# Optimization experiments

Measured on AMD Instinct MI355X. Metric: run time of the kernel, lower is better.

The kernel has to match this reference:

```python
import jax, jax.numpy as jnp
import numpy as np


def _prelu(x, a):
    # torch.nn.PReLU with per-channel parameter a (broadcast over batch)
    return jnp.where(x >= 0, x, a * x)


def setup_inputs() -> dict:
    key = jax.random.key(0)
    ks = jax.random.split(key, 12)
    B = 8192
    dims = [512, 1024, 1024, 512]  # tardim
    E = 8                          # tctrl = modim[-1]
    scale = 0.02                   # keep activations well-scaled across 3 layers
    inp = {
        "x": jax.random.normal(ks[0], (B, dims[0]), dtype=jnp.float32),
        "weights": jax.random.uniform(ks[1], (E,), dtype=jnp.float32),
    }
    for i in range(3):
        din, dout = dims[i], dims[i + 1]
        inp[f"W{i}"] = jax.random.normal(ks[2 + 3 * i], (E, din, dout), dtype=jnp.float32) * scale
        inp[f"b{i}"] = jax.random.normal(ks[3 + 3 * i], (E, dout), dtype=jnp.float32) * scale
        inp[f"a{i}"] = jnp.full((dout,), 0.25, dtype=jnp.float32)  # PReLU init
    return inp


def reference(x, weights, W0, b0, a0, W1, b1, a1, W2, b2, a2):
    # mie.g: per layer, weighted sum over tctrl expert Linears, then PReLU.
    # sum_j (w_j/sum(w)) * (x @ W_j + b_j) == x @ (sum_j wn_j W_j) + sum_j wn_j b_j,
    # so pre-merge expert weights (tiny contraction) and do one GEMM per layer.
    wn = weights / jnp.sum(weights)  # [E]
    for W, b, a in ((W0, b0, a0), (W1, b1, a1), (W2, b2, a2)):
        Wm = jnp.einsum('e,eio->io', wn, W)  # merged weight [in, out]
        bm = jnp.einsum('e,eo->o', wn, b)    # merged bias   [out]
        x = _prelu(x @ Wm + bm, a)           # [B, out]
    return x
```

## Files before the change

kernel.cpp:

```cpp
#include <hip/hip_runtime.h>
#include <stdint.h>

typedef unsigned short u16;
typedef __attribute__((ext_vector_type(8))) short short8;
typedef __attribute__((ext_vector_type(4))) float float4v;

__device__ __forceinline__ u16 f2bf(float f) {
    union { float f; uint32_t u; } v; v.f = f;
    uint32_t r = v.u + 0x7fffu + ((v.u >> 16) & 1u);
    return (u16)(r >> 16);
}

__device__ __forceinline__ void gload16(const u16* g, u16* l) {
    __builtin_amdgcn_global_load_lds(
        (const __attribute__((address_space(1))) void*)g,
        (__attribute__((address_space(3))) void*)l, 16, 0, 0);
}

__global__ __launch_bounds__(256) void prep_fused(
    const float* __restrict__ x, u16* __restrict__ xbf,
    const float* __restrict__ wts,
    const float* __restrict__ W0, const float* __restrict__ W1, const float* __restrict__ W2,
    u16* __restrict__ W0t, u16* __restrict__ W1t, u16* __restrict__ W2t,
    const float* __restrict__ b0, const float* __restrict__ b1, const float* __restrict__ b2,
    float* __restrict__ bm) {
    __shared__ float tile[32][33];
    const int b = blockIdx.x, tid = threadIdx.x;

    if (b < 4096) {
        int i = (b * 256 + tid) * 4;
        float4 v = *(const float4*)(x + i);
        union { u16 s[4]; uint64_t q; } o;
        o.s[0] = f2bf(v.x); o.s[1] = f2bf(v.y); o.s[2] = f2bf(v.z); o.s[3] = f2bf(v.w);
        *(uint64_t*)(xbf + i) = o.q;
        return;
    }

    float wn[8]; float s = 0.f;
    #pragma unroll
    for (int e = 0; e < 8; ++e) { wn[e] = wts[e]; s += wn[e]; }
    const float inv = 1.0f / s;

    if (b < 6144) {
        const float* W; u16* Wt; int K, N, lb;
        if (b < 4608)      { W = W0; Wt = W0t; K = 512;  N = 1024; lb = b - 4096; }
        else if (b < 5632) { W = W1; Wt = W1t; K = 1024; N = 1024; lb = b - 4608; }
        else               { W = W2; Wt = W2t; K = 1024; N = 512;  lb = b - 5632; }
        const int ntiles = N >> 5;
        const int o0 = (lb % ntiles) * 32, i0 = (lb / ntiles) * 32;
        const int tx = tid & 31, ty = tid >> 5;
        #pragma unroll
        for (int s4 = 0; s4 < 4; ++s4) {
            int il = ty + s4 * 8;
            float acc = 0.f;
            #pragma unroll
            for (int e = 0; e < 8; ++e)
                acc += wn[e] * W[(size_t)e * K * N + (size_t)(i0 + il) * N + o0 + tx];
            tile[il][tx] = acc * inv;
        }
        __syncthreads();
        #pragma unroll
        for (int s4 = 0; s4 < 4; ++s4) {
            int ol = ty + s4 * 8;
            Wt[(size_t)(o0 + ol) * K + i0 + tx] = f2bf(tile[tx][ol]);
        }
        return;
    }

    int t = (b - 6144) * 256 + tid;
    if (t >= 2560) return;
    const float* bp; int o, stride;
    if (t < 1024)      { bp = b0; o = t;        stride = 1024; }
    else if (t < 2048) { bp = b1; o = t - 1024; stride = 1024; }
    else               { bp = b2; o = t - 2048; stride = 512;  }
    float acc = 0.f;
    #pragma unroll
    for (int e = 0; e < 8; ++e) acc += wn[e] * bp[e * stride + o];
    bm[t] = acc * inv;
}

template <bool OUT_F32>
__global__ __launch_bounds__(256, 4) void gemm_bias_prelu(
    const u16* __restrict__ A, const u16* __restrict__ Bt,
    const float* __restrict__ bias, const float* __restrict__ alpha,
    void* __restrict__ outp, int M, int N, int K) {
    __shared__ __align__(16) u16 As[128 * 64];
    __shared__ __align__(16) u16 Bs[64 * 64];
    const int tid = threadIdx.x;
    const int bn = blockIdx.x, bm = blockIdx.y;

    const int r0 = tid >> 3;
    const int p  = tid & 7;
    const int c  = p ^ (r0 & 7);
    const u16* Ag = A  + (size_t)(bm * 128 + r0) * K + c * 8;
    const u16* Bg = Bt + (size_t)(bn * 64  + r0) * K + c * 8;
    u16* Al = As + tid * 8;
    u16* Bl = Bs + tid * 8;

    const int lane = tid & 63, w = tid >> 6;
    const int wm = (w >> 1) * 64, wncol = (w & 1) * 32;
    const int l16 = lane & 15, quad = lane >> 4;
    const int xr = l16 & 7;
    const short8* As8 = (const short8*)As;
    const short8* Bs8 = (const short8*)Bs;

    float4v acc[4][2] = {};

    const int nk = K >> 6;
    for (int kt = 0; kt < nk; ++kt) {
        #pragma unroll
        for (int it = 0; it < 4; ++it)
            gload16(Ag + (size_t)(it * 32) * K, Al + it * 2048);
        #pragma unroll
        for (int it = 0; it < 2; ++it)
            gload16(Bg + (size_t)(it * 32) * K, Bl + it * 2048);
        __syncthreads();
        #pragma unroll
        for (int kk = 0; kk < 2; ++kk) {
            const int cb = kk * 4;
            short8 af[4], bf[2];
            #pragma unroll
            for (int mi = 0; mi < 4; ++mi)
                af[mi] = As8[(wm + mi * 16 + l16) * 8 + ((cb + quad) ^ xr)];
            #pragma unroll
            for (int ni = 0; ni < 2; ++ni)
                bf[ni] = Bs8[(wncol + ni * 16 + l16) * 8 + ((cb + quad) ^ xr)];
            #pragma unroll
            for (int mi = 0; mi < 4; ++mi)
                #pragma unroll
                for (int ni = 0; ni < 2; ++ni)
                    acc[mi][ni] = __builtin_amdgcn_mfma_f32_16x16x32_bf16(
                        af[mi], bf[ni], acc[mi][ni], 0, 0, 0);
        }
        if (kt + 1 < nk) __syncthreads();
        Ag += 64; Bg += 64;
    }

    const int cbase = bn * 64 + wncol + l16;
    float bv[2], av[2];
    #pragma unroll
    for (int ni = 0; ni < 2; ++ni) { bv[ni] = bias[cbase + ni * 16]; av[ni] = alpha[cbase + ni * 16]; }
    const int rbase = bm * 128 + wm + quad * 4;
    #pragma unroll
    for (int mi = 0; mi < 4; ++mi) {
        #pragma unroll
        for (int reg = 0; reg < 4; ++reg) {
            int r = rbase + mi * 16 + reg;
            #pragma unroll
            for (int ni = 0; ni < 2; ++ni) {
                float v = acc[mi][ni][reg] + bv[ni];
                v = v >= 0.f ? v : av[ni] * v;
                size_t idx = (size_t)r * N + cbase + ni * 16;
                if (OUT_F32) ((float*)outp)[idx] = v;
                else         ((u16*)outp)[idx] = f2bf(v);
            }
        }
    }
}

extern "C" void kernel_launch(void* const* d_in, const int* in_sizes, int n_in,
                              void* d_out, int out_size, void* d_ws, size_t ws_size,
                              hipStream_t stream) {
    const float* x   = (const float*)d_in[0];
    const float* wts = (const float*)d_in[1];
    const float* W0  = (const float*)d_in[2];
    const float* b0  = (const float*)d_in[3];
    const float* a0  = (const float*)d_in[4];
    const float* W1  = (const float*)d_in[5];
    const float* b1  = (const float*)d_in[6];
    const float* a1  = (const float*)d_in[7];
    const float* W2  = (const float*)d_in[8];
    const float* b2  = (const float*)d_in[9];
    const float* a2  = (const float*)d_in[10];
    float* out = (float*)d_out;

    char* ws = (char*)d_ws;
    u16*   xbf  = (u16*)ws;  ws += (size_t)8192 * 512 * 2;
    u16*   act1 = (u16*)ws;  ws += (size_t)8192 * 1024 * 2;
    u16*   act2 = (u16*)ws;  ws += (size_t)8192 * 1024 * 2;
    u16*   W0t  = (u16*)ws;  ws += (size_t)1024 * 512 * 2;
    u16*   W1t  = (u16*)ws;  ws += (size_t)1024 * 1024 * 2;
    u16*   W2t  = (u16*)ws;  ws += (size_t)512 * 1024 * 2;
    float* bm   = (float*)ws;

    prep_fused<<<6154, 256, 0, stream>>>(x, xbf, wts, W0, W1, W2, W0t, W1t, W2t,
                                         b0, b1, b2, bm);

    gemm_bias_prelu<false><<<dim3(16, 64), 256, 0, stream>>>(xbf,  W0t, bm,        a0, act1, 8192, 1024, 512);
    gemm_bias_prelu<false><<<dim3(16, 64), 256, 0, stream>>>(act1, W1t, bm + 1024, a1, act2, 8192, 1024, 1024);
    gemm_bias_prelu<true ><<<dim3(8, 64),  256, 0, stream>>>(act2, W2t, bm + 2048, a2, out,  8192, 512, 1024);
}
```

Measured before the change: 196.4 us.

## Fuse prep and three GEMM layers into one cooperative persistent kernel

Replaces the four separate launches with a single cooperative kernel of 512 blocks that runs the prep phase and then the three GEMM layers, separated by grid-wide syncs. GEMM tiles grow to 128x128 with 512 threads, so one block covers one output tile per layer and no work loop is needed. This is meant to remove launch gaps and tail effects between kernels. In exchange, a fixed grid of 512 gives exactly one wave with no load balancing, layer 3 leaves half the blocks idle, and the prep phase now runs on far fewer blocks. A non-cooperative fallback path is kept.

```diff
diff --git a/kernel.cpp b/kernel.cpp
--- a/kernel.cpp
+++ b/kernel.cpp
@@ -1,5 +1,8 @@
 #include <hip/hip_runtime.h>
+#include <hip/hip_cooperative_groups.h>
 #include <stdint.h>
+
+namespace cg = cooperative_groups;
 
 typedef unsigned short u16;
 typedef __attribute__((ext_vector_type(8))) short short8;
@@ -17,88 +20,82 @@
         (__attribute__((address_space(3))) void*)l, 16, 0, 0);
 }
 
-__global__ __launch_bounds__(256) void prep_fused(
-    const float* __restrict__ x, u16* __restrict__ xbf,
-    const float* __restrict__ wts,
-    const float* __restrict__ W0, const float* __restrict__ W1, const float* __restrict__ W2,
-    u16* __restrict__ W0t, u16* __restrict__ W1t, u16* __restrict__ W2t,
-    const float* __restrict__ b0, const float* __restrict__ b1, const float* __restrict__ b2,
-    float* __restrict__ bm) {
-    __shared__ float tile[32][33];
-    const int b = blockIdx.x, tid = threadIdx.x;
-
-    if (b < 4096) {
-        int i = (b * 256 + tid) * 4;
-        float4 v = *(const float4*)(x + i);
+struct Params {
+    const float *x, *wts, *W0, *b0, *a0, *W1, *b1, *a1, *W2, *b2, *a2;
+    u16 *xbf, *act1, *act2, *W0t, *W1t, *W2t;
+    float *mb;
+    float *out;
+};
+
+__device__ void prep_phase(const Params& p, int bid, int tid, float (*tile)[33]) {
+    for (int i = (bid * 512 + tid) * 4; i < 8192 * 512; i += 512 * 512 * 4) {
+        float4 v = *(const float4*)(p.x + i);
         union { u16 s[4]; uint64_t q; } o;
         o.s[0] = f2bf(v.x); o.s[1] = f2bf(v.y); o.s[2] = f2bf(v.z); o.s[3] = f2bf(v.w);
-        *(uint64_t*)(xbf + i) = o.q;
-        return;
-    }
-
-    float wn[8]; float s = 0.f;
+        *(uint64_t*)(p.xbf + i) = o.q;
+    }
+
+    float wnv[8]; float ssum = 0.f;
     #pragma unroll
-    for (int e = 0; e < 8; ++e) { wn[e] = wts[e]; s += wn[e]; }
-    const float inv = 1.0f / s;
-
-    if (b < 6144) {
+    for (int e = 0; e < 8; ++e) { wnv[e] = p.wts[e]; ssum += wnv[e]; }
+    const float inv = 1.0f / ssum;
+
+    for (int u = bid; u < 2048; u += 512) {
         const float* W; u16* Wt; int K, N, lb;
-        if (b < 4608)      { W = W0; Wt = W0t; K = 512;  N = 1024; lb = b - 4096; }
-        else if (b < 5632) { W = W1; Wt = W1t; K = 1024; N = 1024; lb = b - 4608; }
-        else               { W = W2; Wt = W2t; K = 1024; N = 512;  lb = b - 5632; }
-        const int ntiles = N >> 5;
-        const int o0 = (lb % ntiles) * 32, i0 = (lb / ntiles) * 32;
+        if (u < 512)       { W = p.W0; Wt = p.W0t; K = 512;  N = 1024; lb = u; }
+        else if (u < 1536) { W = p.W1; Wt = p.W1t; K = 1024; N = 1024; lb = u - 512; }
+        else               { W = p.W2; Wt = p.W2t; K = 1024; N = 512;  lb = u - 1536; }
+        const int nt = N >> 5;
+        const int o0 = (lb % nt) * 32, i0 = (lb / nt) * 32;
         const int tx = tid & 31, ty = tid >> 5;
-        #pragma unroll
-        for (int s4 = 0; s4 < 4; ++s4) {
-            int il = ty + s4 * 8;
+        __syncthreads();
+        #pragma unroll
+        for (int s4 = 0; s4 < 2; ++s4) {
+            int il = ty + s4 * 16;
             float acc = 0.f;
             #pragma unroll
             for (int e = 0; e < 8; ++e)
-                acc += wn[e] * W[(size_t)e * K * N + (size_t)(i0 + il) * N + o0 + tx];
+                acc += wnv[e] * W[(size_t)e * K * N + (size_t)(i0 + il) * N + o0 + tx];
             tile[il][tx] = acc * inv;
         }
         __syncthreads();
         #pragma unroll
-        for (int s4 = 0; s4 < 4; ++s4) {
-            int ol = ty + s4 * 8;
+        for (int s4 = 0; s4 < 2; ++s4) {
+            int ol = ty + s4 * 16;
             Wt[(size_t)(o0 + ol) * K + i0 + tx] = f2bf(tile[tx][ol]);
         }
-        return;
-    }
-
-    int t = (b - 6144) * 256 + tid;
-    if (t >= 2560) return;
-    const float* bp; int o, stride;
-    if (t < 1024)      { bp = b0; o = t;        stride = 1024; }
-    else if (t < 2048) { bp = b1; o = t - 1024; stride = 1024; }
-    else               { bp = b2; o = t - 2048; stride = 512;  }
-    float acc = 0.f;
-    #pragma unroll
-    for (int e = 0; e < 8; ++e) acc += wn[e] * bp[e * stride + o];
-    bm[t] = acc * inv;
+    }
+
+    if (bid < 5) {
+        int t = bid * 512 + tid;
+        if (t < 2560) {
+            const float* bp; int o, stride;
+            if (t < 1024)      { bp = p.b0; o = t;        stride = 1024; }
+            else if (t < 2048) { bp = p.b1; o = t - 1024; stride = 1024; }
+            else               { bp = p.b2; o = t - 2048; stride = 512;  }
+            float acc = 0.f;
+            #pragma unroll
+            for (int e = 0; e < 8; ++e) acc += wnv[e] * bp[e * stride + o];
+            p.mb[t] = acc * inv;
+        }
+    }
 }
 
 template <bool OUT_F32>
-__global__ __launch_bounds__(256, 4) void gemm_bias_prelu(
-    const u16* __restrict__ A, const u16* __restrict__ Bt,
-    const float* __restrict__ bias, const float* __restrict__ alpha,
-    void* __restrict__ outp, int M, int N, int K) {
-    __shared__ __align__(16) u16 As[128 * 64];
-    __shared__ __align__(16) u16 Bs[64 * 64];
-    const int tid = threadIdx.x;
-    const int bn = blockIdx.x, bm = blockIdx.y;
-
+__device__ void gemm_tile(const u16* __restrict__ A, const u16* __restrict__ Bt,
+                          const float* __restrict__ bias, const float* __restrict__ alpha,
+                          void* __restrict__ outp, int N, int K, int bn, int bmi,
+                          u16* As, u16* Bs, int tid) {
     const int r0 = tid >> 3;
     const int p  = tid & 7;
     const int c  = p ^ (r0 & 7);
-    const u16* Ag = A  + (size_t)(bm * 128 + r0) * K + c * 8;
-    const u16* Bg = Bt + (size_t)(bn * 64  + r0) * K + c * 8;
+    const u16* Ag = A  + (size_t)(bmi * 128 + r0) * K + c * 8;
+    const u16* Bg = Bt + (size_t)(bn * 128 + r0) * K + c * 8;
     u16* Al = As + tid * 8;
     u16* Bl = Bs + tid * 8;
 
     const int lane = tid & 63, w = tid >> 6;
-    const int wm = (w >> 1) * 64, wncol = (w & 1) * 32;
+    const int wm = (w >> 2) * 64, wn = (w & 3) * 32;
     const int l16 = lane & 15, quad = lane >> 4;
     const int xr = l16 & 7;
     const short8* As8 = (const short8*)As;
@@ -108,12 +105,10 @@
 
     const int nk = K >> 6;
     for (int kt = 0; kt < nk; ++kt) {
-        #pragma unroll
-        for (int it = 0; it < 4; ++it)
-            gload16(Ag + (size_t)(it * 32) * K, Al + it * 2048);
-        #pragma unroll
-        for (int it = 0; it < 2; ++it)
-            gload16(Bg + (size_t)(it * 32) * K, Bl + it * 2048);
+        gload16(Ag, Al);
+        gload16(Ag + (size_t)64 * K, Al + 4096);
+        gload16(Bg, Bl);
+        gload16(Bg + (size_t)64 * K, Bl + 4096);
         __syncthreads();
         #pragma unroll
         for (int kk = 0; kk < 2; ++kk) {
@@ -124,7 +119,7 @@
                 af[mi] = As8[(wm + mi * 16 + l16) * 8 + ((cb + quad) ^ xr)];
             #pragma unroll
             for (int ni = 0; ni < 2; ++ni)
-                bf[ni] = Bs8[(wncol + ni * 16 + l16) * 8 + ((cb + quad) ^ xr)];
+                bf[ni] = Bs8[(wn + ni * 16 + l16) * 8 + ((cb + quad) ^ xr)];
             #pragma unroll
             for (int mi = 0; mi < 4; ++mi)
                 #pragma unroll
@@ -132,15 +127,15 @@
                     acc[mi][ni] = __builtin_amdgcn_mfma_f32_16x16x32_bf16(
                         af[mi], bf[ni], acc[mi][ni], 0, 0, 0);
         }
-        if (kt + 1 < nk) __syncthreads();
+        __syncthreads();
         Ag += 64; Bg += 64;
     }
 
-    const int cbase = bn * 64 + wncol + l16;
+    const int cbase = bn * 128 + wn + l16;
     float bv[2], av[2];
     #pragma unroll
     for (int ni = 0; ni < 2; ++ni) { bv[ni] = bias[cbase + ni * 16]; av[ni] = alpha[cbase + ni * 16]; }
-    const int rbase = bm * 128 + wm + quad * 4;
+    const int rbase = bmi * 128 + wm + quad * 4;
     #pragma unroll
     for (int mi = 0; mi < 4; ++mi) {
         #pragma unroll
@@ -158,22 +153,47 @@
     }
 }
 
+__global__ __launch_bounds__(512, 4) void fused(Params p) {
+    __shared__ __align__(16) u16 smem[2 * 128 * 64];
+    const int tid = threadIdx.x, bid = blockIdx.x;
+    cg::grid_group grid = cg::this_grid();
+
+    prep_phase(p, bid, tid, (float(*)[33])smem);
+    __threadfence();
+    grid.sync();
+
+    u16* As = smem;
+    u16* Bs = smem + 128 * 64;
+
+    gemm_tile<false>(p.xbf, p.W0t, p.mb, p.a0, p.act1, 1024, 512, bid >> 6, bid & 63, As, Bs, tid);
+    __threadfence();
+    grid.sync();
+
+    gemm_tile<false>(p.act1, p.W1t, p.mb + 1024, p.a1, p.act2, 1024, 1024, bid >> 6, bid & 63, As, Bs, tid);
+    __threadfence();
+    grid.sync();
+
+    if (bid < 256)
+        gemm_tile<true>(p.act2, p.W2t, p.mb + 2048, p.a2, p.out, 512, 1024, bid >> 6, bid & 63, As, Bs, tid);
+}
+
+__global__ __launch_bounds__(512) void prep_k(Params p) {
+    __shared__ float tile[32][33];
+    prep_phase(p, blockIdx.x, threadIdx.x, tile);
+}
+
+template <bool OUT_F32>
+__global__ __launch_bounds__(512, 4) void gemm_k(const u16* __restrict__ A, const u16* __restrict__ Bt,
+                                                 const float* __restrict__ bias, const float* __restrict__ alpha,
+                                                 void* __restrict__ outp, int N, int K) {
+    __shared__ __align__(16) u16 smem[2 * 128 * 64];
+    gemm_tile<OUT_F32>(A, Bt, bias, alpha, outp, N, K, blockIdx.x >> 6, blockIdx.x & 63,
+                       smem, smem + 128 * 64, threadIdx.x);
+}
+
 extern "C" void kernel_launch(void* const* d_in, const int* in_sizes, int n_in,
                               void* d_out, int out_size, void* d_ws, size_t ws_size,
                               hipStream_t stream) {
-    const float* x   = (const float*)d_in[0];
-    const float* wts = (const float*)d_in[1];
-    const float* W0  = (const float*)d_in[2];
-    const float* b0  = (const float*)d_in[3];
-    const float* a0  = (const float*)d_in[4];
-    const float* W1  = (const float*)d_in[5];
-    const float* b1  = (const float*)d_in[6];
-    const float* a1  = (const float*)d_in[7];
-    const float* W2  = (const float*)d_in[8];
-    const float* b2  = (const float*)d_in[9];
-    const float* a2  = (const float*)d_in[10];
-    float* out = (float*)d_out;
-
     char* ws = (char*)d_ws;
     u16*   xbf  = (u16*)ws;  ws += (size_t)8192 * 512 * 2;
     u16*   act1 = (u16*)ws;  ws += (size_t)8192 * 1024 * 2;
@@ -181,12 +201,33 @@
     u16*   W0t  = (u16*)ws;  ws += (size_t)1024 * 512 * 2;
     u16*   W1t  = (u16*)ws;  ws += (size_t)1024 * 1024 * 2;
     u16*   W2t  = (u16*)ws;  ws += (size_t)512 * 1024 * 2;
-    float* bm   = (float*)ws;
-
-    prep_fused<<<6154, 256, 0, stream>>>(x, xbf, wts, W0, W1, W2, W0t, W1t, W2t,
-                                         b0, b1, b2, bm);
-
-    gemm_bias_prelu<false><<<dim3(16, 64), 256, 0, stream>>>(xbf,  W0t, bm,        a0, act1, 8192, 1024, 512);
-    gemm_bias_prelu<false><<<dim3(16, 64), 256, 0, stream>>>(act1, W1t, bm + 1024, a1, act2, 8192, 1024, 1024);
-    gemm_bias_prelu<true ><<<dim3(8, 64),  256, 0, stream>>>(act2, W2t, bm + 2048, a2, out,  8192, 512, 1024);
-}
+    float* mb   = (float*)ws;
+
+    Params prm;
+    prm.x   = (const float*)d_in[0];
+    prm.wts = (const float*)d_in[1];
+    prm.W0  = (const float*)d_in[2];
+    prm.b0  = (const float*)d_in[3];
+    prm.a0  = (const float*)d_in[4];
+    prm.W1  = (const float*)d_in[5];
+    prm.b1  = (const float*)d_in[6];
+    prm.a1  = (const float*)d_in[7];
+    prm.W2  = (const float*)d_in[8];
+    prm.b2  = (const float*)d_in[9];
+    prm.a2  = (const float*)d_in[10];
+    prm.xbf = xbf; prm.act1 = act1; prm.act2 = act2;
+    prm.W0t = W0t; prm.W1t = W1t; prm.W2t = W2t;
+    prm.mb  = mb;
+    prm.out = (float*)d_out;
+
+    void* args[] = { (void*)&prm };
+    hipError_t e = hipLaunchCooperativeKernel((const void*)fused, dim3(512), dim3(512),
+                                              args, 0, stream);
+    if (e != hipSuccess) {
+        (void)hipGetLastError();
+        prep_k<<<512, 512, 0, stream>>>(prm);
+        gemm_k<false><<<512, 512, 0, stream>>>(xbf,  W0t, mb,        prm.a0, act1, 1024, 512);
+        gemm_k<false><<<512, 512, 0, stream>>>(act1, W1t, mb + 1024, prm.a1, act2, 1024, 1024);
+        gemm_k<true ><<<256, 512, 0, stream>>>(act2, W2t, mb + 2048, prm.a2, prm.out, 512, 1024);
+    }
+}
```

New measurement: 719.2 us. +266.1%, slower.

## Enlarge GEMM tile to 128x128 and remap blocks for XCD-local L2 reuse

Applied to the files above, without the earlier changes.

Doubles the N-tile from 64 to 128 so each wave computes a 64x64 output (4x4 MFMA accumulators), raising arithmetic intensity per LDS load. Blocks now use a 1D grid, remapped so that each XCD (blockIdx & 7) handles a contiguous band of row tiles, keeping A rows and B tiles shared within one L2. The costs are more registers, loss of the occupancy hint in launch bounds, and fewer blocks (512/256) relative to CU count, which may leave the last layer under-filling the GPU.

```diff
diff --git a/kernel.cpp b/kernel.cpp
--- a/kernel.cpp
+++ b/kernel.cpp
@@ -79,56 +79,59 @@
     bm[t] = acc * inv;
 }
 
-template <bool OUT_F32>
-__global__ __launch_bounds__(256, 4) void gemm_bias_prelu(
+template <bool OUT_F32, int NN_LOG2>
+__global__ __launch_bounds__(256) void gemm_bias_prelu(
     const u16* __restrict__ A, const u16* __restrict__ Bt,
     const float* __restrict__ bias, const float* __restrict__ alpha,
     void* __restrict__ outp, int M, int N, int K) {
     __shared__ __align__(16) u16 As[128 * 64];
-    __shared__ __align__(16) u16 Bs[64 * 64];
+    __shared__ __align__(16) u16 Bs[128 * 64];
     const int tid = threadIdx.x;
-    const int bn = blockIdx.x, bm = blockIdx.y;
+
+    const int xcd   = blockIdx.x & 7;
+    const int inner = blockIdx.x >> 3;
+    const int bn    = inner & ((1 << NN_LOG2) - 1);
+    const int bmv   = xcd * 8 + (inner >> NN_LOG2);
 
     const int r0 = tid >> 3;
     const int p  = tid & 7;
     const int c  = p ^ (r0 & 7);
-    const u16* Ag = A  + (size_t)(bm * 128 + r0) * K + c * 8;
-    const u16* Bg = Bt + (size_t)(bn * 64  + r0) * K + c * 8;
+    const u16* Ag = A  + (size_t)(bmv * 128 + r0) * K + c * 8;
+    const u16* Bg = Bt + (size_t)(bn * 128 + r0) * K + c * 8;
     u16* Al = As + tid * 8;
     u16* Bl = Bs + tid * 8;
 
     const int lane = tid & 63, w = tid >> 6;
-    const int wm = (w >> 1) * 64, wncol = (w & 1) * 32;
+    const int wm = (w >> 1) * 64, wn = (w & 1) * 64;
     const int l16 = lane & 15, quad = lane >> 4;
     const int xr = l16 & 7;
     const short8* As8 = (const short8*)As;
     const short8* Bs8 = (const short8*)Bs;
 
-    float4v acc[4][2] = {};
+    float4v acc[4][4] = {};
 
     const int nk = K >> 6;
     for (int kt = 0; kt < nk; ++kt) {
         #pragma unroll
-        for (int it = 0; it < 4; ++it)
+        for (int it = 0; it < 4; ++it) {
             gload16(Ag + (size_t)(it * 32) * K, Al + it * 2048);
-        #pragma unroll
-        for (int it = 0; it < 2; ++it)
             gload16(Bg + (size_t)(it * 32) * K, Bl + it * 2048);
+        }
         __syncthreads();
         #pragma unroll
         for (int kk = 0; kk < 2; ++kk) {
             const int cb = kk * 4;
-            short8 af[4], bf[2];
+            short8 af[4], bf[4];
             #pragma unroll
             for (int mi = 0; mi < 4; ++mi)
                 af[mi] = As8[(wm + mi * 16 + l16) * 8 + ((cb + quad) ^ xr)];
             #pragma unroll
-            for (int ni = 0; ni < 2; ++ni)
-                bf[ni] = Bs8[(wncol + ni * 16 + l16) * 8 + ((cb + quad) ^ xr)];
+            for (int ni = 0; ni < 4; ++ni)
+                bf[ni] = Bs8[(wn + ni * 16 + l16) * 8 + ((cb + quad) ^ xr)];
             #pragma unroll
             for (int mi = 0; mi < 4; ++mi)
                 #pragma unroll
-                for (int ni = 0; ni < 2; ++ni)
+                for (int ni = 0; ni < 4; ++ni)
                     acc[mi][ni] = __builtin_amdgcn_mfma_f32_16x16x32_bf16(
                         af[mi], bf[ni], acc[mi][ni], 0, 0, 0);
         }
@@ -136,18 +139,18 @@
         Ag += 64; Bg += 64;
     }
 
-    const int cbase = bn * 64 + wncol + l16;
-    float bv[2], av[2];
+    const int cbase = bn * 128 + wn + l16;
+    float bv[4], av[4];
     #pragma unroll
-    for (int ni = 0; ni < 2; ++ni) { bv[ni] = bias[cbase + ni * 16]; av[ni] = alpha[cbase + ni * 16]; }
-    const int rbase = bm * 128 + wm + quad * 4;
+    for (int ni = 0; ni < 4; ++ni) { bv[ni] = bias[cbase + ni * 16]; av[ni] = alpha[cbase + ni * 16]; }
+    const int rbase = bmv * 128 + wm + quad * 4;
     #pragma unroll
     for (int mi = 0; mi < 4; ++mi) {
         #pragma unroll
         for (int reg = 0; reg < 4; ++reg) {
             int r = rbase + mi * 16 + reg;
             #pragma unroll
-            for (int ni = 0; ni < 2; ++ni) {
+            for (int ni = 0; ni < 4; ++ni) {
                 float v = acc[mi][ni][reg] + bv[ni];
                 v = v >= 0.f ? v : av[ni] * v;
                 size_t idx = (size_t)r * N + cbase + ni * 16;
@@ -186,7 +189,7 @@
     prep_fused<<<6154, 256, 0, stream>>>(x, xbf, wts, W0, W1, W2, W0t, W1t, W2t,
                                          b0, b1, b2, bm);
 
-    gemm_bias_prelu<false><<<dim3(16, 64), 256, 0, stream>>>(xbf,  W0t, bm,        a0, act1, 8192, 1024, 512);
-    gemm_bias_prelu<false><<<dim3(16, 64), 256, 0, stream>>>(act1, W1t, bm + 1024, a1, act2, 8192, 1024, 1024);
-    gemm_bias_prelu<true ><<<dim3(8, 64),  256, 0, stream>>>(act2, W2t, bm + 2048, a2, out,  8192, 512, 1024);
+    gemm_bias_prelu<false, 3><<<512, 256, 0, stream>>>(xbf,  W0t, bm,        a0, act1, 8192, 1024, 512);
+    gemm_bias_prelu<false, 3><<<512, 256, 0, stream>>>(act1, W1t, bm + 1024, a1, act2, 8192, 1024, 1024);
+    gemm_bias_prelu<true,  2><<<256, 256, 0, stream>>>(act2, W2t, bm + 2048, a2, out,  8192, 512, 1024);
 }
```

New measurement: 196.8 us. No clear change (+0.2%).
